# Kernel optimization log

Hardware: AMD Instinct MI355X
Metric: run time of the kernel (lower is better)

The kernel has to match this reference:

```python
import jax, jax.numpy as jnp
import numpy as np
import math

B, N, D, H, FFN = 64, 128, 128, 4, 128
NEG = -9e15
LRELU_SLOPE = 0.2  # LeakyReLU alpha from init_kwargs


def entmax_bisect(x, alpha, n_iter=30):
    # alpha-entmax via bisection (entmax package algorithm); alpha broadcastable, in (1, 2].
    am1 = alpha - 1.0
    x = x * am1
    d = x.shape[-1]
    max_val = jnp.max(x, axis=-1, keepdims=True)
    tau_lo = max_val - 1.0
    tau_hi = max_val - (1.0 / d) ** am1

    def p(tau):
        return jnp.maximum(x - tau, 0.0) ** (1.0 / am1)

    f_lo = jnp.sum(p(tau_lo), axis=-1, keepdims=True) - 1.0
    for _ in range(n_iter):  # fixed iteration count -> jit friendly
        tau_m = 0.5 * (tau_lo + tau_hi)
        f_m = jnp.sum(p(tau_m), axis=-1, keepdims=True) - 1.0
        same = (f_m * f_lo) >= 0
        tau_lo = jnp.where(same, tau_m, tau_lo)
        f_lo = jnp.where(same, f_m, f_lo)
        tau_hi = jnp.where(same, tau_hi, tau_m)
    pm = p(0.5 * (tau_lo + tau_hi))
    return pm / jnp.sum(pm, axis=-1, keepdims=True)


def layernorm(x, g, b, eps=1e-5):
    mu = jnp.mean(x, axis=-1, keepdims=True)
    var = jnp.var(x, axis=-1, keepdims=True)
    return (x - mu) / jnp.sqrt(var + eps) * g + b


def setup_inputs() -> dict:
    key = jax.random.key(0)
    ks = jax.random.split(key, 24)
    s = 0.05
    sw = 1.0 / math.sqrt(D)
    return {
        "hidden": jax.random.normal(ks[0], (B, N, D), jnp.float32),
        "adj": jax.random.randint(ks[1], (B, N, N), 0, 5, jnp.int32),
        "a0": jax.random.normal(ks[2], (D,), jnp.float32) * s,
        "a1": jax.random.normal(ks[3], (D,), jnp.float32) * s,
        "a2": jax.random.normal(ks[4], (D,), jnp.float32) * s,
        "a3": jax.random.normal(ks[5], (D,), jnp.float32) * s,
        "wa": jax.random.normal(ks[6], (D, 1), jnp.float32) * s,
        "ba": jnp.zeros((1,), jnp.float32),
        "wq": jax.random.normal(ks[7], (D, D), jnp.float32) * sw,
        "bq": jnp.zeros((D,), jnp.float32),
        "wk": jax.random.normal(ks[8], (D, D), jnp.float32) * sw,
        "bk": jnp.zeros((D,), jnp.float32),
        "wv": jax.random.normal(ks[9], (D, D), jnp.float32) * sw,
        "bv": jnp.zeros((D,), jnp.float32),
        "w1": jax.random.normal(ks[10], (D, FFN), jnp.float32) * sw,
        "b1": jnp.zeros((FFN,), jnp.float32),
        "w2": jax.random.normal(ks[11], (FFN, D), jnp.float32) * sw,
        "b2": jnp.zeros((D,), jnp.float32),
        "ln_g": jnp.ones((D,), jnp.float32),
        "ln_b": jnp.zeros((D,), jnp.float32),
        "seq_mask": jnp.ones((B, N), jnp.int32),
        "num_heads": H,
    }


def reference(hidden, adj, a0, a1, a2, a3, wa, ba, wq, bq, wk, bk, wv, bv,
              w1, b1, w2, b2, ln_g, ln_b, seq_mask, num_heads):
    Bs, Ns, Ds = hidden.shape
    hd = Ds // num_heads
    # ---- LocalAggregator: relation-typed graph attention (4 edge types) ----
    # e_r[b,i,j] = leakyrelu(sum_d h[b,i,d]*h[b,j,d]*a_r[d]); same math as the
    # original B x N x N x dim repeat/view/matmul, expressed as one contraction.
    A = jnp.stack([a0, a1, a2, a3], axis=1)  # [D, 4]
    e = jax.nn.leaky_relu(jnp.einsum('bid,bjd,dr->bijr', hidden, hidden, A),
                          LRELU_SLOPE)  # [B, N, N, 4]
    att = jnp.full((Bs, Ns, Ns), NEG, dtype=hidden.dtype)
    for r in range(4):  # adj value r+1 selects relation r (original torch.where order)
        att = jnp.where(adj == r + 1, e[..., r], att)
    att = jax.nn.softmax(att, axis=-1)
    local = jnp.einsum('bij,bjd->bid', att, hidden)  # [B, N, D]
    # ---- get_alpha(flag=3): per-session entmax alpha from last position ----
    a_ent = jax.nn.sigmoid(local[:, -1] @ wa + ba) + 1.0  # [B, 1]
    a_ent = jnp.where(a_ent == 1.0, 1.00001, a_ent)
    a_ent = a_ent[:, :, None, None]  # [B,1,1,1] broadcasts over heads/rows/cols
    # ---- EncoderLayer with entmax-bisect multi-head attention (sparse=True) ----
    q = (local @ wq + bq).reshape(Bs, Ns, num_heads, hd).transpose(0, 2, 1, 3)
    k = (local @ wk + bk).reshape(Bs, Ns, num_heads, hd).transpose(0, 2, 1, 3)
    v = (local @ wv + bv).reshape(Bs, Ns, num_heads, hd).transpose(0, 2, 1, 3)
    scores = jnp.einsum('bhid,bhjd->bhij', q, k) / math.sqrt(Ds)  # note: sqrt(dim), as in source
    scores = jnp.where(seq_mask[:, None, None, :] == 0, -1e9, scores)
    alpha = entmax_bisect(scores, a_ent)
    y = jnp.einsum('bhij,bhjd->bhid', alpha, v)
    y = y.transpose(0, 2, 1, 3).reshape(Bs, Ns, Ds)  # output_layer NOT applied (as in source)
    x = local + y
    y2 = jax.nn.relu(y @ w1 + b1) @ w2 + b2  # FFN applied to y, not x (as in source)
    x = x + y2
    return layernorm(x, ln_g, ln_b)
```

## Files before the change

### kernel.cpp

```cpp
#include <hip/hip_runtime.h>
#include <math.h>

#define BB 64
#define NN 128
#define DD 128
#define HH 4
#define HD 32
#define FFN_ 128

static constexpr float NEGV  = -9000000000000000.0f;
static constexpr float SLOPE = 0.2f;
static constexpr float SCALE = 0.08838834764831845f;
#define NEWTON_ITERS 5

__device__ __forceinline__ float4 f4fma(float s, float4 w, float4 a) {
    a.x += s * w.x; a.y += s * w.y; a.z += s * w.z; a.w += s * w.w; return a;
}

__global__ __launch_bounds__(512) void k_att_local(
    const float* __restrict__ hidden, const int* __restrict__ adj,
    const float* __restrict__ a0, const float* __restrict__ a1,
    const float* __restrict__ a2, const float* __restrict__ a3,
    const float* __restrict__ wa, const float* __restrict__ ba,
    float* __restrict__ local, float* __restrict__ aent_out)
{
    __shared__ __align__(16) float At[4][132];
    __shared__ __align__(16) float hb[128][128];
    __shared__ __align__(16) float att[16][132];

    const int blk = blockIdx.x;
    const int b  = blk >> 3;
    const int i0 = (blk & 7) * 16;
    const int tid = threadIdx.x;

    {
        int r = tid >> 7, d = tid & 127;
        float v = (r == 0) ? a0[d] : (r == 1) ? a1[d] : (r == 2) ? a2[d] : a3[d];
        At[r][d] = v;
    }
    #pragma unroll
    for (int p = 0; p < 8; ++p) {
        int q = tid + 512 * p;
        int r = q >> 5, cq = q & 31;
        *reinterpret_cast<float4*>(&hb[r][4 * (cq ^ (r >> 2))]) =
            *reinterpret_cast<const float4*>(&hidden[(size_t)b * NN * DD + (size_t)r * DD + 4 * cq]);
    }
    __syncthreads();

    {
        const int ig = tid >> 7;
        const int j  = tid & 127;
        const int ib = 4 * ig;
        int a0i = adj[(size_t)b * NN * NN + (size_t)(i0 + ib + 0) * NN + j];
        int a1i = adj[(size_t)b * NN * NN + (size_t)(i0 + ib + 1) * NN + j];
        int a2i = adj[(size_t)b * NN * NN + (size_t)(i0 + ib + 2) * NN + j];
        int a3i = adj[(size_t)b * NN * NN + (size_t)(i0 + ib + 3) * NN + j];
        bool v0 = (a0i >= 1 && a0i <= 4), v1 = (a1i >= 1 && a1i <= 4);
        bool v2 = (a2i >= 1 && a2i <= 4), v3 = (a3i >= 1 && a3i <= 4);
        int r0 = v0 ? (a0i - 1) : 0, r1 = v1 ? (a1i - 1) : 0;
        int r2 = v2 ? (a2i - 1) : 0, r3 = v3 ? (a3i - 1) : 0;
        const int jx = j >> 2;
        const int h0x = (i0 + ib + 0) >> 2, h1x = (i0 + ib + 1) >> 2;
        const int h2x = (i0 + ib + 2) >> 2, h3x = (i0 + ib + 3) >> 2;
        float acc0 = 0.0f, acc1 = 0.0f, acc2 = 0.0f, acc3 = 0.0f;
        #pragma unroll 4
        for (int dq = 0; dq < 32; ++dq) {
            float4 jv = *reinterpret_cast<const float4*>(&hb[j][4 * (dq ^ jx)]);
            float4 h0 = *reinterpret_cast<const float4*>(&hb[i0 + ib + 0][4 * (dq ^ h0x)]);
            float4 h1 = *reinterpret_cast<const float4*>(&hb[i0 + ib + 1][4 * (dq ^ h1x)]);
            float4 h2 = *reinterpret_cast<const float4*>(&hb[i0 + ib + 2][4 * (dq ^ h2x)]);
            float4 h3 = *reinterpret_cast<const float4*>(&hb[i0 + ib + 3][4 * (dq ^ h3x)]);
            float4 A0 = *reinterpret_cast<const float4*>(&At[r0][4 * dq]);
            float4 A1 = *reinterpret_cast<const float4*>(&At[r1][4 * dq]);
            float4 A2 = *reinterpret_cast<const float4*>(&At[r2][4 * dq]);
            float4 A3 = *reinterpret_cast<const float4*>(&At[r3][4 * dq]);
            acc0 += (h0.x * jv.x) * A0.x + (h0.y * jv.y) * A0.y + (h0.z * jv.z) * A0.z + (h0.w * jv.w) * A0.w;
            acc1 += (h1.x * jv.x) * A1.x + (h1.y * jv.y) * A1.y + (h1.z * jv.z) * A1.z + (h1.w * jv.w) * A1.w;
            acc2 += (h2.x * jv.x) * A2.x + (h2.y * jv.y) * A2.y + (h2.z * jv.z) * A2.z + (h2.w * jv.w) * A2.w;
            acc3 += (h3.x * jv.x) * A3.x + (h3.y * jv.y) * A3.y + (h3.z * jv.z) * A3.z + (h3.w * jv.w) * A3.w;
        }
        float e0 = (acc0 > 0.0f) ? acc0 : SLOPE * acc0;
        float e1 = (acc1 > 0.0f) ? acc1 : SLOPE * acc1;
        float e2 = (acc2 > 0.0f) ? acc2 : SLOPE * acc2;
        float e3 = (acc3 > 0.0f) ? acc3 : SLOPE * acc3;
        att[ib + 0][j] = v0 ? e0 : NEGV;
        att[ib + 1][j] = v1 ? e1 : NEGV;
        att[ib + 2][j] = v2 ? e2 : NEGV;
        att[ib + 3][j] = v3 ? e3 : NEGV;
    }
    __syncthreads();

    const int ti = tid >> 5;
    const int tl = tid & 31;

    {
        float x0 = att[ti][tl], x1 = att[ti][tl + 32], x2 = att[ti][tl + 64], x3 = att[ti][tl + 96];
        float m = fmaxf(fmaxf(x0, x1), fmaxf(x2, x3));
        #pragma unroll
        for (int off = 16; off >= 1; off >>= 1) m = fmaxf(m, __shfl_xor(m, off));
        float q0 = __expf(x0 - m), q1 = __expf(x1 - m), q2 = __expf(x2 - m), q3 = __expf(x3 - m);
        float s = (q0 + q1) + (q2 + q3);
        #pragma unroll
        for (int off = 16; off >= 1; off >>= 1) s += __shfl_xor(s, off);
        float invs = 1.0f / s;
        att[ti][tl]      = q0 * invs;
        att[ti][tl + 32] = q1 * invs;
        att[ti][tl + 64] = q2 * invs;
        att[ti][tl + 96] = q3 * invs;
    }

    const int jg = 4 * tl;
    float4 acc4 = make_float4(0.0f, 0.0f, 0.0f, 0.0f);
    #pragma unroll 4
    for (int jq = 0; jq < 32; ++jq) {
        int xc = 4 * (tl ^ jq);
        #pragma unroll
        for (int k = 0; k < 4; ++k) {
            int j = 4 * jq + k;
            float av = att[ti][j];
            float4 h4 = *reinterpret_cast<const float4*>(&hb[j][xc]);
            acc4.x += av * h4.x; acc4.y += av * h4.y;
            acc4.z += av * h4.z; acc4.w += av * h4.w;
        }
    }
    *reinterpret_cast<float4*>(&local[(size_t)b * NN * DD + (size_t)(i0 + ti) * DD + jg]) = acc4;

    if (((blk & 7) == 7) && ti == 15) {
        float4 wa4 = *reinterpret_cast<const float4*>(&wa[jg]);
        float dp = acc4.x * wa4.x + acc4.y * wa4.y + acc4.z * wa4.z + acc4.w * wa4.w;
        #pragma unroll
        for (int off = 16; off >= 1; off >>= 1) dp += __shfl_xor(dp, off, 32);
        if (tl == 0) {
            float z = dp + ba[0];
            float sig = 1.0f / (1.0f + __expf(-z));
            float a = sig + 1.0f;
            if (a == 1.0f) a = 1.00001f;
            aent_out[b] = a;
        }
    }
}

__global__ __launch_bounds__(1024) void k_qkv_entmax(
    const float* __restrict__ local,
    const float* __restrict__ wq, const float* __restrict__ bq,
    const float* __restrict__ wk, const float* __restrict__ bk,
    const float* __restrict__ wv, const float* __restrict__ bv,
    const float* __restrict__ aent, const int* __restrict__ seq_mask,
    float* __restrict__ y)
{
    __shared__ __align__(16) float lb[128][132];
    __shared__ __align__(16) float wQs[128][36];
    __shared__ __align__(16) float wKs[128][36];
    __shared__ __align__(16) float wVs[128][36];
    __shared__ __align__(16) float kx[32][132];
    __shared__ __align__(16) float vL[128][32];
    __shared__ int maskL[NN];
    __shared__ float aent_sh;

    const int blk = blockIdx.x;
    const int b = blk >> 2, h = blk & 3;
    const int tid = threadIdx.x;

    #pragma unroll
    for (int p = 0; p < 4; ++p) {
        int idx = tid + 1024 * p;
        int r = idx >> 5, cq = idx & 31;
        *reinterpret_cast<float4*>(&lb[r][4 * cq]) =
            *reinterpret_cast<const float4*>(&local[(size_t)b * NN * DD + (size_t)r * DD + 4 * cq]);
    }
    {
        int d = tid >> 3, c4 = 4 * (tid & 7);
        size_t off = (size_t)d * DD + h * HD + c4;
        *reinterpret_cast<float4*>(&wQs[d][c4]) = *reinterpret_cast<const float4*>(&wq[off]);
        *reinterpret_cast<float4*>(&wKs[d][c4]) = *reinterpret_cast<const float4*>(&wk[off]);
        *reinterpret_cast<float4*>(&wVs[d][c4]) = *reinterpret_cast<const float4*>(&wv[off]);
    }
    if (tid < NN) maskL[tid] = seq_mask[b * NN + tid];
    if (tid == 0) aent_sh = aent[b];
    __syncthreads();

    if (tid < 512) {
        const int rp = tid >> 3;
        const int tx = tid & 7;
        const int cg = 4 * tx;
        const int r0 = 2 * rp, r1 = 2 * rp + 1;

        float4 qb4 = *reinterpret_cast<const float4*>(&bq[h * HD + cg]);
        float4 kb4 = *reinterpret_cast<const float4*>(&bk[h * HD + cg]);
        float4 vb4 = *reinterpret_cast<const float4*>(&bv[h * HD + cg]);
        float4 qa0 = qb4, qa1 = qb4;
        float4 ka0 = kb4, ka1 = kb4;
        float4 va0 = vb4, va1 = vb4;

        #pragma unroll 4
        for (int kq = 0; kq < 32; ++kq) {
            float4 a0 = *reinterpret_cast<const float4*>(&lb[r0][4 * kq]);
            float4 a1 = *reinterpret_cast<const float4*>(&lb[r1][4 * kq]);
            {
                float4 w0 = *reinterpret_cast<const float4*>(&wQs[4 * kq + 0][cg]);
                float4 w1 = *reinterpret_cast<const float4*>(&wQs[4 * kq + 1][cg]);
                float4 w2 = *reinterpret_cast<const float4*>(&wQs[4 * kq + 2][cg]);
                float4 w3 = *reinterpret_cast<const float4*>(&wQs[4 * kq + 3][cg]);
                qa0 = f4fma(a0.x, w0, qa0); qa0 = f4fma(a0.y, w1, qa0);
                qa0 = f4fma(a0.z, w2, qa0); qa0 = f4fma(a0.w, w3, qa0);
                qa1 = f4fma(a1.x, w0, qa1); qa1 = f4fma(a1.y, w1, qa1);
                qa1 = f4fma(a1.z, w2, qa1); qa1 = f4fma(a1.w, w3, qa1);
            }
            {
                float4 w0 = *reinterpret_cast<const float4*>(&wKs[4 * kq + 0][cg]);
                float4 w1 = *reinterpret_cast<const float4*>(&wKs[4 * kq + 1][cg]);
                float4 w2 = *reinterpret_cast<const float4*>(&wKs[4 * kq + 2][cg]);
                float4 w3 = *reinterpret_cast<const float4*>(&wKs[4 * kq + 3][cg]);
                ka0 = f4fma(a0.x, w0, ka0); ka0 = f4fma(a0.y, w1, ka0);
                ka0 = f4fma(a0.z, w2, ka0); ka0 = f4fma(a0.w, w3, ka0);
                ka1 = f4fma(a1.x, w0, ka1); ka1 = f4fma(a1.y, w1, ka1);
                ka1 = f4fma(a1.z, w2, ka1); ka1 = f4fma(a1.w, w3, ka1);
            }
            {
                float4 w0 = *reinterpret_cast<const float4*>(&wVs[4 * kq + 0][cg]);
                float4 w1 = *reinterpret_cast<const float4*>(&wVs[4 * kq + 1][cg]);
                float4 w2 = *reinterpret_cast<const float4*>(&wVs[4 * kq + 2][cg]);
                float4 w3 = *reinterpret_cast<const float4*>(&wVs[4 * kq + 3][cg]);
                va0 = f4fma(a0.x, w0, va0); va0 = f4fma(a0.y, w1, va0);
                va0 = f4fma(a0.z, w2, va0); va0 = f4fma(a0.w, w3, va0);
                va1 = f4fma(a1.x, w0, va1); va1 = f4fma(a1.y, w1, va1);
                va1 = f4fma(a1.z, w2, va1); va1 = f4fma(a1.w, w3, va1);
            }
        }
        kx[cg + 0][r0] = ka0.x; kx[cg + 1][r0] = ka0.y;
        kx[cg + 2][r0] = ka0.z; kx[cg + 3][r0] = ka0.w;
        kx[cg + 0][r1] = ka1.x; kx[cg + 1][r1] = ka1.y;
        kx[cg + 2][r1] = ka1.z; kx[cg + 3][r1] = ka1.w;
        *reinterpret_cast<float4*>(&vL[r0][cg]) = va0;
        *reinterpret_cast<float4*>(&vL[r1][cg]) = va1;
        *reinterpret_cast<float4*>(&lb[r0][cg]) = qa0;
        *reinterpret_cast<float4*>(&lb[r1][cg]) = qa1;
    }
    __syncthreads();

    if (tid < 512) {
        const int rp  = tid >> 3;
        const int sub = tid & 7;
        const int c0  = 4 * sub;
        const int iA  = rp, iB = rp + 64;

        const float am1 = aent_sh - 1.0f;
        const float inv = 1.0f / am1;
        const float invm1 = inv - 1.0f;
        const float thi_off = exp2f(-7.0f * am1);
        const float sc = SCALE * am1;
        const float xneg = -1000000000.0f * am1;

        float xvA[16], xvB[16];
        #pragma unroll
        for (int s = 0; s < 16; ++s) { xvA[s] = 0.0f; xvB[s] = 0.0f; }
        #pragma unroll
        for (int dq = 0; dq < 8; ++dq) {
            float4 qA = *reinterpret_cast<const float4*>(&lb[iA][4 * dq]);
            float4 qB = *reinterpret_cast<const float4*>(&lb[iB][4 * dq]);
            #pragma unroll
            for (int kk = 0; kk < 4; ++kk) {
                int dh = 4 * dq + kk;
                float qa = (kk == 0) ? qA.x : (kk == 1) ? qA.y : (kk == 2) ? qA.z : qA.w;
                float qb = (kk == 0) ? qB.x : (kk == 1) ? qB.y : (kk == 2) ? qB.z : qB.w;
                #pragma unroll
                for (int qq = 0; qq < 4; ++qq) {
                    float4 k4 = *reinterpret_cast<const float4*>(&kx[dh][c0 + 32 * qq]);
                    xvA[4 * qq + 0] += qa * k4.x;  xvB[4 * qq + 0] += qb * k4.x;
                    xvA[4 * qq + 1] += qa * k4.y;  xvB[4 * qq + 1] += qb * k4.y;
                    xvA[4 * qq + 2] += qa * k4.z;  xvB[4 * qq + 2] += qb * k4.z;
                    xvA[4 * qq + 3] += qa * k4.w;  xvB[4 * qq + 3] += qb * k4.w;
                }
            }
        }
        #pragma unroll
        for (int qq = 0; qq < 4; ++qq) {
            int4 m4 = *reinterpret_cast<const int4*>(&maskL[c0 + 32 * qq]);
            xvA[4 * qq + 0] = (m4.x == 0) ? xneg : xvA[4 * qq + 0] * sc;
            xvA[4 * qq + 1] = (m4.y == 0) ? xneg : xvA[4 * qq + 1] * sc;
            xvA[4 * qq + 2] = (m4.z == 0) ? xneg : xvA[4 * qq + 2] * sc;
            xvA[4 * qq + 3] = (m4.w == 0) ? xneg : xvA[4 * qq + 3] * sc;
            xvB[4 * qq + 0] = (m4.x == 0) ? xneg : xvB[4 * qq + 0] * sc;
            xvB[4 * qq + 1] = (m4.y == 0) ? xneg : xvB[4 * qq + 1] * sc;
            xvB[4 * qq + 2] = (m4.z == 0) ? xneg : xvB[4 * qq + 2] * sc;
            xvB[4 * qq + 3] = (m4.w == 0) ? xneg : xvB[4 * qq + 3] * sc;
        }

        float mxA = xvA[0], mxB = xvB[0];
        #pragma unroll
        for (int s = 1; s < 16; ++s) { mxA = fmaxf(mxA, xvA[s]); mxB = fmaxf(mxB, xvB[s]); }
        mxA = fmaxf(mxA, __shfl_xor(mxA, 1)); mxB = fmaxf(mxB, __shfl_xor(mxB, 1));
        mxA = fmaxf(mxA, __shfl_xor(mxA, 2)); mxB = fmaxf(mxB, __shfl_xor(mxB, 2));
        mxA = fmaxf(mxA, __shfl_xor(mxA, 4)); mxB = fmaxf(mxB, __shfl_xor(mxB, 4));

        const float hiA = mxA - thi_off, hiB = mxB - thi_off;
        float tauA = mxA - 1.0f, tauB = mxB - 1.0f;

        #pragma unroll
        for (int it = 0; it < NEWTON_ITERS; ++it) {
            float psA = 0.0f, dsA = 0.0f, psB = 0.0f, dsB = 0.0f;
            #pragma unroll
            for (int s = 0; s < 16; ++s) {
                float tA = fmaxf(xvA[s] - tauA, 0.0f);
                float lA = __builtin_amdgcn_logf(tA);
                float dA = __builtin_amdgcn_exp2f(invm1 * lA);
                float pA = tA * dA;
                psA += pA; dsA += dA;
                float tB = fmaxf(xvB[s] - tauB, 0.0f);
                float lB = __builtin_amdgcn_logf(tB);
                float dB = __builtin_amdgcn_exp2f(invm1 * lB);
                float pB = tB * dB;
                psB += pB; dsB += dB;
            }
            psA += __shfl_xor(psA, 1); dsA += __shfl_xor(dsA, 1);
            psA += __shfl_xor(psA, 2); dsA += __shfl_xor(dsA, 2);
            psA += __shfl_xor(psA, 4); dsA += __shfl_xor(dsA, 4);
            psB += __shfl_xor(psB, 1); dsB += __shfl_xor(dsB, 1);
            psB += __shfl_xor(psB, 2); dsB += __shfl_xor(dsB, 2);
            psB += __shfl_xor(psB, 4); dsB += __shfl_xor(dsB, 4);
            tauA = fminf(tauA + (psA - 1.0f) * __builtin_amdgcn_rcpf(inv * dsA), hiA);
            tauB = fminf(tauB + (psB - 1.0f) * __builtin_amdgcn_rcpf(inv * dsB), hiB);
        }

        {
            float pm[16]; float S = 0.0f;
            #pragma unroll
            for (int s = 0; s < 16; ++s) {
                float t = fmaxf(xvA[s] - tauA, 0.0f);
                float l = __builtin_amdgcn_logf(t);
                float p = t * __builtin_amdgcn_exp2f(invm1 * l);
                pm[s] = p; S += p;
            }
            S += __shfl_xor(S, 1); S += __shfl_xor(S, 2); S += __shfl_xor(S, 4);
            float invS = __builtin_amdgcn_rcpf(S);
            #pragma unroll
            for (int qq = 0; qq < 4; ++qq) {
                float4 a4 = make_float4(pm[4 * qq + 0] * invS, pm[4 * qq + 1] * invS,
                                        pm[4 * qq + 2] * invS, pm[4 * qq + 3] * invS);
                *reinterpret_cast<float4*>(&lb[iA][c0 + 32 * qq]) = a4;
            }
        }
        {
            float pm[16]; float S = 0.0f;
            #pragma unroll
            for (int s = 0; s < 16; ++s) {
                float t = fmaxf(xvB[s] - tauB, 0.0f);
                float l = __builtin_amdgcn_logf(t);
                float p = t * __builtin_amdgcn_exp2f(invm1 * l);
                pm[s] = p; S += p;
            }
            S += __shfl_xor(S, 1); S += __shfl_xor(S, 2); S += __shfl_xor(S, 4);
            float invS = __builtin_amdgcn_rcpf(S);
            #pragma unroll
            for (int qq = 0; qq < 4; ++qq) {
                float4 a4 = make_float4(pm[4 * qq + 0] * invS, pm[4 * qq + 1] * invS,
                                        pm[4 * qq + 2] * invS, pm[4 * qq + 3] * invS);
                *reinterpret_cast<float4*>(&lb[iB][c0 + 32 * qq]) = a4;
            }
        }

        float4 accA = make_float4(0.0f, 0.0f, 0.0f, 0.0f);
        float4 accB = make_float4(0.0f, 0.0f, 0.0f, 0.0f);
        #pragma unroll 4
        for (int q2 = 0; q2 < 32; ++q2) {
            float4 aA = *reinterpret_cast<const float4*>(&lb[iA][4 * q2]);
            float4 aB = *reinterpret_cast<const float4*>(&lb[iB][4 * q2]);
            float4 v0 = *reinterpret_cast<const float4*>(&vL[4 * q2 + 0][c0]);
            float4 v1 = *reinterpret_cast<const float4*>(&vL[4 * q2 + 1][c0]);
            float4 v2 = *reinterpret_cast<const float4*>(&vL[4 * q2 + 2][c0]);
            float4 v3 = *reinterpret_cast<const float4*>(&vL[4 * q2 + 3][c0]);
            accA.x += aA.x * v0.x + aA.y * v1.x + aA.z * v2.x + aA.w * v3.x;
            accA.y += aA.x * v0.y + aA.y * v1.y + aA.z * v2.y + aA.w * v3.y;
            accA.z += aA.x * v0.z + aA.y * v1.z + aA.z * v2.z + aA.w * v3.z;
            accA.w += aA.x * v0.w + aA.y * v1.w + aA.z * v2.w + aA.w * v3.w;
            accB.x += aB.x * v0.x + aB.y * v1.x + aB.z * v2.x + aB.w * v3.x;
            accB.y += aB.x * v0.y + aB.y * v1.y + aB.z * v2.y + aB.w * v3.y;
            accB.z += aB.x * v0.z + aB.y * v1.z + aB.z * v2.z + aB.w * v3.z;
            accB.w += aB.x * v0.w + aB.y * v1.w + aB.z * v2.w + aB.w * v3.w;
        }
        *reinterpret_cast<float4*>(&y[(size_t)b * NN * DD + (size_t)iA * DD + h * HD + c0]) = accA;
        *reinterpret_cast<float4*>(&y[(size_t)b * NN * DD + (size_t)iB * DD + h * HD + c0]) = accB;
    }
}

__global__ __launch_bounds__(512) void k_ffn_ln(
    const float* __restrict__ yv, const float* __restrict__ w1,
    const float* __restrict__ b1, const float* __restrict__ w2,
    const float* __restrict__ b2, const float* __restrict__ local,
    const float* __restrict__ g, const float* __restrict__ bb,
    float* __restrict__ out)
{
    __shared__ __align__(16) float Bs[128][128];
    __shared__ __align__(16) float As[32][128];
    __shared__ __align__(16) float Zs[32][128];
    const int mt = blockIdx.x;
    const int b  = mt >> 2;
    const int i0 = (mt & 3) * 32;
    const int tid = threadIdx.x;

    #pragma unroll
    for (int p = 0; p < 8; ++p) {
        int idx = tid + 512 * p;
        int d = idx >> 5, cq = idx & 31;
        *reinterpret_cast<float4*>(&Bs[d][4 * cq]) =
            *reinterpret_cast<const float4*>(&w1[d * FFN_ + 4 * cq]);
    }
    #pragma unroll
    for (int p = 0; p < 2; ++p) {
        int idx = tid + 512 * p;
        int row = idx >> 5, kq = idx & 31;
        *reinterpret_cast<float4*>(&As[row][4 * kq]) =
            *reinterpret_cast<const float4*>(&yv[(size_t)b * NN * DD + (size_t)(i0 + row) * DD + 4 * kq]);
    }
    __syncthreads();

    const int tx = tid & 31, ty = tid >> 5;
    const int c0 = 4 * tx;

    {
        float4 bias = *reinterpret_cast<const float4*>(&b1[c0]);
        float acc[2][4];
        #pragma unroll
        for (int i = 0; i < 2; ++i)
            #pragma unroll
            for (int j = 0; j < 4; ++j) acc[i][j] = 0.0f;
        #pragma unroll 2
        for (int kq = 0; kq < 32; ++kq) {
            float4 b0 = *reinterpret_cast<const float4*>(&Bs[4 * kq + 0][c0]);
            float4 b1v = *reinterpret_cast<const float4*>(&Bs[4 * kq + 1][c0]);
            float4 b2v = *reinterpret_cast<const float4*>(&Bs[4 * kq + 2][c0]);
            float4 b3v = *reinterpret_cast<const float4*>(&Bs[4 * kq + 3][c0]);
            #pragma unroll
            for (int i = 0; i < 2; ++i) {
                float4 a = *reinterpret_cast<const float4*>(&As[2 * ty + i][4 * kq]);
                acc[i][0] += a.x * b0.x + a.y * b1v.x + a.z * b2v.x + a.w * b3v.x;
                acc[i][1] += a.x * b0.y + a.y * b1v.y + a.z * b2v.y + a.w * b3v.y;
                acc[i][2] += a.x * b0.z + a.y * b1v.z + a.z * b2v.z + a.w * b3v.z;
                acc[i][3] += a.x * b0.w + a.y * b1v.w + a.z * b2v.w + a.w * b3v.w;
            }
        }
        #pragma unroll
        for (int i = 0; i < 2; ++i) {
            *reinterpret_cast<float4*>(&Zs[2 * ty + i][c0]) =
                make_float4(fmaxf(acc[i][0] + bias.x, 0.0f), fmaxf(acc[i][1] + bias.y, 0.0f),
                            fmaxf(acc[i][2] + bias.z, 0.0f), fmaxf(acc[i][3] + bias.w, 0.0f));
        }
    }
    __syncthreads();

    #pragma unroll
    for (int p = 0; p < 8; ++p) {
        int idx = tid + 512 * p;
        int d = idx >> 5, cq = idx & 31;
        *reinterpret_cast<float4*>(&Bs[d][4 * cq]) =
            *reinterpret_cast<const float4*>(&w2[d * DD + 4 * cq]);
    }
    __syncthreads();

    float4 bias = *reinterpret_cast<const float4*>(&b2[c0]);
    float4 g4 = *reinterpret_cast<const float4*>(&g[c0]);
    float4 bb4 = *reinterpret_cast<const float4*>(&bb[c0]);
    float acc[2][4];
    #pragma unroll
    for (int i = 0; i < 2; ++i)
        #pragma unroll
        for (int j = 0; j < 4; ++j) acc[i][j] = 0.0f;
    #pragma unroll 2
    for (int kq = 0; kq < 32; ++kq) {
        float4 b0 = *reinterpret_cast<const float4*>(&Bs[4 * kq + 0][c0]);
        float4 b1v = *reinterpret_cast<const float4*>(&Bs[4 * kq + 1][c0]);
        float4 b2v = *reinterpret_cast<const float4*>(&Bs[4 * kq + 2][c0]);
        float4 b3v = *reinterpret_cast<const float4*>(&Bs[4 * kq + 3][c0]);
        #pragma unroll
        for (int i = 0; i < 2; ++i) {
            float4 a = *reinterpret_cast<const float4*>(&Zs[2 * ty + i][4 * kq]);
            acc[i][0] += a.x * b0.x + a.y * b1v.x + a.z * b2v.x + a.w * b3v.x;
            acc[i][1] += a.x * b0.y + a.y * b1v.y + a.z * b2v.y + a.w * b3v.y;
            acc[i][2] += a.x * b0.z + a.y * b1v.z + a.z * b2v.z + a.w * b3v.z;
            acc[i][3] += a.x * b0.w + a.y * b1v.w + a.z * b2v.w + a.w * b3v.w;
        }
    }

    #pragma unroll
    for (int i = 0; i < 2; ++i) {
        size_t base = (size_t)b * NN * DD + (size_t)(i0 + 2 * ty + i) * DD + c0;
        float4 l4 = *reinterpret_cast<const float4*>(&local[base]);
        float4 y4 = *reinterpret_cast<const float4*>(&yv[base]);
        float x0 = acc[i][0] + bias.x + l4.x + y4.x;
        float x1 = acc[i][1] + bias.y + l4.y + y4.y;
        float x2 = acc[i][2] + bias.z + l4.z + y4.z;
        float x3 = acc[i][3] + bias.w + l4.w + y4.w;

        float s = (x0 + x1) + (x2 + x3);
        s += __shfl_xor(s, 1); s += __shfl_xor(s, 2); s += __shfl_xor(s, 4);
        s += __shfl_xor(s, 8); s += __shfl_xor(s, 16);
        float mu = s * (1.0f / 128.0f);
        float d0 = x0 - mu, d1 = x1 - mu, d2 = x2 - mu, d3 = x3 - mu;
        float v = (d0 * d0 + d1 * d1) + (d2 * d2 + d3 * d3);
        v += __shfl_xor(v, 1); v += __shfl_xor(v, 2); v += __shfl_xor(v, 4);
        v += __shfl_xor(v, 8); v += __shfl_xor(v, 16);
        float rstd = rsqrtf(v * (1.0f / 128.0f) + 1e-5f);
        float4 o = make_float4(d0 * rstd * g4.x + bb4.x, d1 * rstd * g4.y + bb4.y,
                               d2 * rstd * g4.z + bb4.z, d3 * rstd * g4.w + bb4.w);
        *reinterpret_cast<float4*>(&out[base]) = o;
    }
}

extern "C" void kernel_launch(void* const* d_in, const int* in_sizes, int n_in,
                              void* d_out, int out_size, void* d_ws, size_t ws_size,
                              hipStream_t stream) {
    const float* hidden = (const float*)d_in[0];
    const int*   adj    = (const int*)d_in[1];
    const float* a0 = (const float*)d_in[2];
    const float* a1 = (const float*)d_in[3];
    const float* a2 = (const float*)d_in[4];
    const float* a3 = (const float*)d_in[5];
    const float* wa = (const float*)d_in[6];
    const float* ba = (const float*)d_in[7];
    const float* wq = (const float*)d_in[8];
    const float* bq = (const float*)d_in[9];
    const float* wk = (const float*)d_in[10];
    const float* bk = (const float*)d_in[11];
    const float* wv = (const float*)d_in[12];
    const float* bv = (const float*)d_in[13];
    const float* w1 = (const float*)d_in[14];
    const float* b1 = (const float*)d_in[15];
    const float* w2 = (const float*)d_in[16];
    const float* b2 = (const float*)d_in[17];
    const float* g  = (const float*)d_in[18];
    const float* bb = (const float*)d_in[19];
    const int* seq_mask = (const int*)d_in[20];

    float* ws   = (float*)d_ws;
    float* local = ws;
    float* yv    = ws + 1048576;
    float* aentw = ws + 2 * 1048576;
    float* out   = (float*)d_out;

    k_att_local<<<dim3(512), dim3(512), 0, stream>>>(hidden, adj, a0, a1, a2, a3,
                                                     wa, ba, local, aentw);
    k_qkv_entmax<<<dim3(256), dim3(1024), 0, stream>>>(local, wq, bq, wk, bk, wv, bv,
                                                       aentw, seq_mask, yv);
    k_ffn_ln<<<dim3(256), dim3(512), 0, stream>>>(yv, w1, b1, w2, b2, local, g, bb, out);
}
```

Baseline: 74.55 us.

## Precompute h*A products in shared memory and split QKV projection across thread halves

```diff
diff --git a/kernel.cpp b/kernel.cpp
--- a/kernel.cpp
+++ b/kernel.cpp
@@ -26,6 +26,7 @@
 {
     __shared__ __align__(16) float At[4][132];
     __shared__ __align__(16) float hb[128][128];
+    __shared__ __align__(16) float hA[64][132];
     __shared__ __align__(16) float att[16][132];
 
     const int blk = blockIdx.x;
@@ -44,6 +45,19 @@
         int r = q >> 5, cq = q & 31;
         *reinterpret_cast<float4*>(&hb[r][4 * (cq ^ (r >> 2))]) =
             *reinterpret_cast<const float4*>(&hidden[(size_t)b * NN * DD + (size_t)r * DD + 4 * cq]);
+    }
+    __syncthreads();
+
+    #pragma unroll
+    for (int p = 0; p < 4; ++p) {
+        int idx = tid + 512 * p;
+        int i  = idx >> 7;
+        int r  = (idx >> 5) & 3;
+        int dq = idx & 31;
+        float4 hv = *reinterpret_cast<const float4*>(&hb[i0 + i][4 * (dq ^ ((i0 + i) >> 2))]);
+        float4 av = *reinterpret_cast<const float4*>(&At[r][4 * dq]);
+        *reinterpret_cast<float4*>(&hA[i * 4 + r][4 * dq]) =
+            make_float4(hv.x * av.x, hv.y * av.y, hv.z * av.z, hv.w * av.w);
     }
     __syncthreads();
 
@@ -60,24 +74,22 @@
         int r0 = v0 ? (a0i - 1) : 0, r1 = v1 ? (a1i - 1) : 0;
         int r2 = v2 ? (a2i - 1) : 0, r3 = v3 ? (a3i - 1) : 0;
         const int jx = j >> 2;
-        const int h0x = (i0 + ib + 0) >> 2, h1x = (i0 + ib + 1) >> 2;
-        const int h2x = (i0 + ib + 2) >> 2, h3x = (i0 + ib + 3) >> 2;
+        const int row0 = (ib + 0) * 4 + r0;
+        const int row1 = (ib + 1) * 4 + r1;
+        const int row2 = (ib + 2) * 4 + r2;
+        const int row3 = (ib + 3) * 4 + r3;
         float acc0 = 0.0f, acc1 = 0.0f, acc2 = 0.0f, acc3 = 0.0f;
         #pragma unroll 4
         for (int dq = 0; dq < 32; ++dq) {
             float4 jv = *reinterpret_cast<const float4*>(&hb[j][4 * (dq ^ jx)]);
-            float4 h0 = *reinterpret_cast<const float4*>(&hb[i0 + ib + 0][4 * (dq ^ h0x)]);
-            float4 h1 = *reinterpret_cast<const float4*>(&hb[i0 + ib + 1][4 * (dq ^ h1x)]);
-            float4 h2 = *reinterpret_cast<const float4*>(&hb[i0 + ib + 2][4 * (dq ^ h2x)]);
-            float4 h3 = *reinterpret_cast<const float4*>(&hb[i0 + ib + 3][4 * (dq ^ h3x)]);
-            float4 A0 = *reinterpret_cast<const float4*>(&At[r0][4 * dq]);
-            float4 A1 = *reinterpret_cast<const float4*>(&At[r1][4 * dq]);
-            float4 A2 = *reinterpret_cast<const float4*>(&At[r2][4 * dq]);
-            float4 A3 = *reinterpret_cast<const float4*>(&At[r3][4 * dq]);
-            acc0 += (h0.x * jv.x) * A0.x + (h0.y * jv.y) * A0.y + (h0.z * jv.z) * A0.z + (h0.w * jv.w) * A0.w;
-            acc1 += (h1.x * jv.x) * A1.x + (h1.y * jv.y) * A1.y + (h1.z * jv.z) * A1.z + (h1.w * jv.w) * A1.w;
-            acc2 += (h2.x * jv.x) * A2.x + (h2.y * jv.y) * A2.y + (h2.z * jv.z) * A2.z + (h2.w * jv.w) * A2.w;
-            acc3 += (h3.x * jv.x) * A3.x + (h3.y * jv.y) * A3.y + (h3.z * jv.z) * A3.z + (h3.w * jv.w) * A3.w;
+            float4 A0 = *reinterpret_cast<const float4*>(&hA[row0][4 * dq]);
+            float4 A1 = *reinterpret_cast<const float4*>(&hA[row1][4 * dq]);
+            float4 A2 = *reinterpret_cast<const float4*>(&hA[row2][4 * dq]);
+            float4 A3 = *reinterpret_cast<const float4*>(&hA[row3][4 * dq]);
+            acc0 += A0.x * jv.x + A0.y * jv.y + A0.z * jv.z + A0.w * jv.w;
+            acc1 += A1.x * jv.x + A1.y * jv.y + A1.z * jv.z + A1.w * jv.w;
+            acc2 += A2.x * jv.x + A2.y * jv.y + A2.z * jv.z + A2.w * jv.w;
+            acc3 += A3.x * jv.x + A3.y * jv.y + A3.z * jv.z + A3.w * jv.w;
         }
         float e0 = (acc0 > 0.0f) ? acc0 : SLOPE * acc0;
         float e1 = (acc1 > 0.0f) ? acc1 : SLOPE * acc1;
@@ -179,33 +191,21 @@
     if (tid == 0) aent_sh = aent[b];
     __syncthreads();
 
+    const int t512 = tid & 511;
+    const int rp = t512 >> 3;
+    const int txg = t512 & 7;
+    const int cg = 4 * txg;
+    const int r0 = 2 * rp, r1 = 2 * rp + 1;
+    float4 qa0, qa1;
+
     if (tid < 512) {
-        const int rp = tid >> 3;
-        const int tx = tid & 7;
-        const int cg = 4 * tx;
-        const int r0 = 2 * rp, r1 = 2 * rp + 1;
-
-        float4 qb4 = *reinterpret_cast<const float4*>(&bq[h * HD + cg]);
         float4 kb4 = *reinterpret_cast<const float4*>(&bk[h * HD + cg]);
         float4 vb4 = *reinterpret_cast<const float4*>(&bv[h * HD + cg]);
-        float4 qa0 = qb4, qa1 = qb4;
-        float4 ka0 = kb4, ka1 = kb4;
-        float4 va0 = vb4, va1 = vb4;
-
+        float4 ka0 = kb4, ka1 = kb4, va0 = vb4, va1 = vb4;
         #pragma unroll 4
         for (int kq = 0; kq < 32; ++kq) {
             float4 a0 = *reinterpret_cast<const float4*>(&lb[r0][4 * kq]);
             float4 a1 = *reinterpret_cast<const float4*>(&lb[r1][4 * kq]);
-            {
-                float4 w0 = *reinterpret_cast<const float4*>(&wQs[4 * kq + 0][cg]);
-                float4 w1 = *reinterpret_cast<const float4*>(&wQs[4 * kq + 1][cg]);
-                float4 w2 = *reinterpret_cast<const float4*>(&wQs[4 * kq + 2][cg]);
-                float4 w3 = *reinterpret_cast<const float4*>(&wQs[4 * kq + 3][cg]);
-                qa0 = f4fma(a0.x, w0, qa0); qa0 = f4fma(a0.y, w1, qa0);
-                qa0 = f4fma(a0.z, w2, qa0); qa0 = f4fma(a0.w, w3, qa0);
-                qa1 = f4fma(a1.x, w0, qa1); qa1 = f4fma(a1.y, w1, qa1);
-                qa1 = f4fma(a1.z, w2, qa1); qa1 = f4fma(a1.w, w3, qa1);
-            }
             {
                 float4 w0 = *reinterpret_cast<const float4*>(&wKs[4 * kq + 0][cg]);
                 float4 w1 = *reinterpret_cast<const float4*>(&wKs[4 * kq + 1][cg]);
@@ -233,14 +233,33 @@
         kx[cg + 2][r1] = ka1.z; kx[cg + 3][r1] = ka1.w;
         *reinterpret_cast<float4*>(&vL[r0][cg]) = va0;
         *reinterpret_cast<float4*>(&vL[r1][cg]) = va1;
-        *reinterpret_cast<float4*>(&lb[r0][cg]) = qa0;
-        *reinterpret_cast<float4*>(&lb[r1][cg]) = qa1;
+    } else {
+        float4 qb4 = *reinterpret_cast<const float4*>(&bq[h * HD + cg]);
+        qa0 = qb4; qa1 = qb4;
+        #pragma unroll 4
+        for (int kq = 0; kq < 32; ++kq) {
+            float4 a0 = *reinterpret_cast<const float4*>(&lb[r0][4 * kq]);
+            float4 a1 = *reinterpret_cast<const float4*>(&lb[r1][4 * kq]);
+            float4 w0 = *reinterpret_cast<const float4*>(&wQs[4 * kq + 0][cg]);
+            float4 w1 = *reinterpret_cast<const float4*>(&wQs[4 * kq + 1][cg]);
+            float4 w2 = *reinterpret_cast<const float4*>(&wQs[4 * kq + 2][cg]);
+            float4 w3 = *reinterpret_cast<const float4*>(&wQs[4 * kq + 3][cg]);
+            qa0 = f4fma(a0.x, w0, qa0); qa0 = f4fma(a0.y, w1, qa0);
+            qa0 = f4fma(a0.z, w2, qa0); qa0 = f4fma(a0.w, w3, qa0);
+            qa1 = f4fma(a1.x, w0, qa1); qa1 = f4fma(a1.y, w1, qa1);
+            qa1 = f4fma(a1.z, w2, qa1); qa1 = f4fma(a1.w, w3, qa1);
+        }
+    }
+    __syncthreads();
+
+    if (tid >= 512) {
+        *reinterpret_cast<float4*>(&wQs[r0][cg]) = qa0;
+        *reinterpret_cast<float4*>(&wQs[r1][cg]) = qa1;
     }
     __syncthreads();
 
     if (tid < 512) {
-        const int rp  = tid >> 3;
-        const int sub = tid & 7;
+        const int sub = t512 & 7;
         const int c0  = 4 * sub;
         const int iA  = rp, iB = rp + 64;
 
@@ -256,8 +275,8 @@
         for (int s = 0; s < 16; ++s) { xvA[s] = 0.0f; xvB[s] = 0.0f; }
         #pragma unroll
         for (int dq = 0; dq < 8; ++dq) {
-            float4 qA = *reinterpret_cast<const float4*>(&lb[iA][4 * dq]);
-            float4 qB = *reinterpret_cast<const float4*>(&lb[iB][4 * dq]);
+            float4 qA = *reinterpret_cast<const float4*>(&wQs[iA][4 * dq]);
+            float4 qB = *reinterpret_cast<const float4*>(&wQs[iB][4 * dq]);
             #pragma unroll
             for (int kk = 0; kk < 4; ++kk) {
                 int dh = 4 * dq + kk;
```

Measured after the change: 73.30 us. Within noise of the previous version (-1.7%).
